# Optimization experiments

Hardware: AMD Instinct MI355X
Metric: run time of the kernel (lower is better)

The kernel has to match this reference:

```python
import jax, jax.numpy as jnp
import numpy as np

D_MODEL = 1024
N_HEADS = 16
HEAD_DIM = D_MODEL // N_HEADS


def setup_inputs() -> dict:
    key = jax.random.key(0)
    ks = jax.random.split(key, 5)
    x = jax.random.normal(ks[0], (4, 2048, D_MODEL), dtype=jnp.float32)
    s = 1.0 / np.sqrt(D_MODEL)
    W_qkv = jax.random.normal(ks[1], (D_MODEL, 3 * D_MODEL), dtype=jnp.float32) * s
    b_qkv = jnp.zeros((3 * D_MODEL,), dtype=jnp.float32)
    W_proj = jax.random.normal(ks[2], (D_MODEL, D_MODEL), dtype=jnp.float32) * s
    b_proj = jnp.zeros((D_MODEL,), dtype=jnp.float32)
    return {"x": x, "W_qkv": W_qkv, "b_qkv": b_qkv, "W_proj": W_proj, "b_proj": b_proj}


def reference(x, W_qkv, b_qkv, W_proj, b_proj):
    B, T, C = x.shape
    H, Dh = N_HEADS, HEAD_DIM
    qkv = x @ W_qkv + b_qkv                      # [B,T,3C]
    q, k, v = jnp.split(qkv, 3, axis=-1)
    # [B,T,C] -> [B,H,T,Dh]
    q = q.reshape(B, T, H, Dh).transpose(0, 2, 1, 3)
    k = k.reshape(B, T, H, Dh).transpose(0, 2, 1, 3)
    v = v.reshape(B, T, H, Dh).transpose(0, 2, 1, 3)
    scale = 1.0 / np.sqrt(Dh)
    att = jnp.einsum("bhqd,bhkd->bhqk", q, k) * scale
    causal = jnp.tril(jnp.ones((T, T), dtype=bool))
    att = jnp.where(causal, att, -jnp.inf)
    att = jax.nn.softmax(att, axis=-1)
    y = jnp.einsum("bhqk,bhkd->bhqd", att, v)    # [B,H,T,Dh]
    y = y.transpose(0, 2, 1, 3).reshape(B, T, C)
    return y @ W_proj + b_proj
```

## Files before the change

kernel.cpp:

```cpp
#include <hip/hip_runtime.h>
#include <hip/hip_bf16.h>
#include <cstdint>
#include <math.h>

#define DM   1024
#define NH   16
#define DH   64
#define BB   4
#define TT   2048
#define MTOT (BB*TT)

using short8 = __attribute__((ext_vector_type(8))) short;
using f32x4  = __attribute__((ext_vector_type(4))) float;

__device__ __forceinline__ f32x4 mfma16(short8 a, short8 b, f32x4 c) {
  return __builtin_amdgcn_mfma_f32_16x16x32_bf16(a, b, c, 0, 0, 0);
}

typedef const __attribute__((address_space(1))) unsigned int* as1_u32p;
typedef __attribute__((address_space(3))) unsigned int*       as3_u32p;

__device__ __forceinline__ void gl_lds16(const void* g, void* l) {
  __builtin_amdgcn_global_load_lds(
      (as1_u32p)(reinterpret_cast<uintptr_t>(g)),
      (as3_u32p)((unsigned int)(reinterpret_cast<uintptr_t>(l))),
      16, 0, 0);
}

__device__ __forceinline__ int swz64(int row, int col) {
  return row*64 + ((((col >> 3) ^ (row & 7)) << 3) | (col & 7));
}

__device__ __forceinline__ unsigned pkbf(float a, float b) {
  __hip_bfloat162 h = __float22bfloat162_rn(make_float2(a, b));
  return *reinterpret_cast<unsigned*>(&h);
}

__device__ __forceinline__ void perm16p(unsigned &a, unsigned &b) {
  asm("v_permlane16_swap_b32 %0, %1" : "+v"(a), "+v"(b));
}
__device__ __forceinline__ void perm32p(unsigned &a, unsigned &b) {
  asm("v_permlane32_swap_b32 %0, %1" : "+v"(a), "+v"(b));
}

__device__ __forceinline__ short8 ldsr_o0(unsigned a) {
  short8 r; asm volatile("ds_read_b128 %0, %1" : "=v"(r) : "v"(a)); return r;
}
__device__ __forceinline__ short8 ldsr_o1(unsigned a) {
  short8 r; asm volatile("ds_read_b128 %0, %1 offset:2048" : "=v"(r) : "v"(a)); return r;
}
__device__ __forceinline__ short8 ldsr_o2(unsigned a) {
  short8 r; asm volatile("ds_read_b128 %0, %1 offset:4096" : "=v"(r) : "v"(a)); return r;
}
__device__ __forceinline__ short8 ldsr_o3(unsigned a) {
  short8 r; asm volatile("ds_read_b128 %0, %1 offset:6144" : "=v"(r) : "v"(a)); return r;
}
__device__ __forceinline__ short8 ldsr_o4(unsigned a) {
  short8 r; asm volatile("ds_read_b128 %0, %1 offset:8192" : "=v"(r) : "v"(a)); return r;
}
__device__ __forceinline__ short8 ldsr_o5(unsigned a) {
  short8 r; asm volatile("ds_read_b128 %0, %1 offset:10240" : "=v"(r) : "v"(a)); return r;
}

#define LGKM0  do { asm volatile("s_waitcnt lgkmcnt(0)"); __builtin_amdgcn_sched_barrier(0); } while(0)
#define VMCNT6 do { __builtin_amdgcn_sched_barrier(0); asm volatile("s_waitcnt vmcnt(6)"); __builtin_amdgcn_sched_barrier(0); } while(0)
#define VMCNT0 do { __builtin_amdgcn_sched_barrier(0); asm volatile("s_waitcnt vmcnt(0)"); __builtin_amdgcn_sched_barrier(0); } while(0)
#define BARRIER do { __builtin_amdgcn_s_barrier(); __builtin_amdgcn_sched_barrier(0); } while(0)

__global__ __launch_bounds__(256) void k_cvt(const float* __restrict__ in,
                                             __hip_bfloat16* __restrict__ out, int n8) {
  int i = blockIdx.x * 256 + threadIdx.x;
  if (i >= n8) return;
  const float* p = in + (size_t)i * 8;
  short8 o;
#pragma unroll
  for (int j = 0; j < 8; ++j) {
    __hip_bfloat16 h = __float2bfloat16(p[j]);
    o[j] = *reinterpret_cast<short*>(&h);
  }
  *reinterpret_cast<short8*>(out + (size_t)i * 8) = o;
}

__global__ __launch_bounds__(256) void k_transpose_cvt(const float* __restrict__ W,
                                                       __hip_bfloat16* __restrict__ Wt,
                                                       int K, int N) {
  __shared__ float tbuf[32][33];
  const int n0 = blockIdx.x * 32, k0 = blockIdx.y * 32;
  const int tx = threadIdx.x & 31, ty = threadIdx.x >> 5;
#pragma unroll
  for (int i = 0; i < 4; ++i)
    tbuf[ty + i*8][tx] = W[(size_t)(k0 + ty + i*8) * N + n0 + tx];
  __syncthreads();
#pragma unroll
  for (int i = 0; i < 4; ++i)
    Wt[(size_t)(n0 + ty + i*8) * K + k0 + tx] = __float2bfloat16(tbuf[tx][ty + i*8]);
}

__global__ __launch_bounds__(512, 2) void k_gemm3(const __hip_bfloat16* __restrict__ A,
                                                  const __hip_bfloat16* __restrict__ Bt,
                                                  const float* __restrict__ bias,
                                                  __hip_bfloat16* __restrict__ Qb,
                                                  __hip_bfloat16* __restrict__ Kb,
                                                  __hip_bfloat16* __restrict__ Vtb) {
  __shared__ __hip_bfloat16 As[2][256 * 64];
  __shared__ __hip_bfloat16 Bs[2][192 * 64];
  const int tid = threadIdx.x;
  const int l = tid & 63, w = tid >> 6;
  const int lr = l & 15, lg = l >> 4;
  const int wm = w >> 1, wn = w & 1;
  const int m0 = blockIdx.x * 256, n0 = blockIdx.y * 192;

  const int srow = tid >> 3;
  const int scol = (((tid & 7) ^ (srow & 7)) << 3);
  const size_t aoffs = (size_t)(m0 + srow) * 1024 + scol;
  const size_t boffs = (size_t)(n0 + srow) * 1024 + scol;
  const int ldst = tid * 8;

  auto stage = [&](int t, int s) {
    const int k0 = t * 64;
#pragma unroll
    for (int rd = 0; rd < 4; ++rd)
      gl_lds16(A + aoffs + (size_t)rd * 65536 + k0, &As[s][rd * 4096 + ldst]);
#pragma unroll
    for (int rd = 0; rd < 3; ++rd)
      gl_lds16(Bt + boffs + (size_t)rd * 65536 + k0, &Bs[s][rd * 4096 + ldst]);
  };

  const unsigned asLds = (unsigned)(uintptr_t)&As[0][0];
  const unsigned bsLds = (unsigned)(uintptr_t)&Bs[0][0];
  const unsigned aBase0 = asLds + 2u * ((wm*64 + lr) * 64 + ((lg ^ (lr & 7)) << 3));
  const unsigned bBase0 = bsLds + 2u * ((wn*96 + lr) * 64 + ((lg ^ (lr & 7)) << 3));

  stage(0, 0);
  VMCNT0;
  BARRIER;

  f32x4 acc[4][6] = {};
  short8 a_[4][2], b_[3][2];

#pragma unroll
  for (int t = 0; t < 16; ++t) {
    const int s = t & 1;
    const unsigned aB0 = aBase0 + (unsigned)s * 32768u;
    const unsigned aB1 = aB0 ^ 64u;
    const unsigned bB0 = bBase0 + (unsigned)s * 24576u;
    const unsigned bB1 = bB0 ^ 64u;
    if (t < 15) stage(t + 1, s ^ 1);
    a_[0][0] = ldsr_o0(aB0); a_[1][0] = ldsr_o1(aB0); a_[2][0] = ldsr_o2(aB0); a_[3][0] = ldsr_o3(aB0);
    a_[0][1] = ldsr_o0(aB1); a_[1][1] = ldsr_o1(aB1); a_[2][1] = ldsr_o2(aB1); a_[3][1] = ldsr_o3(aB1);
    b_[0][0] = ldsr_o0(bB0); b_[1][0] = ldsr_o1(bB0); b_[2][0] = ldsr_o2(bB0);
    b_[0][1] = ldsr_o0(bB1); b_[1][1] = ldsr_o1(bB1); b_[2][1] = ldsr_o2(bB1);
    LGKM0;
    __builtin_amdgcn_s_setprio(1);
#pragma unroll
    for (int m = 0; m < 4; ++m)
#pragma unroll
      for (int n = 0; n < 3; ++n)
#pragma unroll
        for (int ks = 0; ks < 2; ++ks)
          acc[m][n] = mfma16(a_[m][ks], b_[n][ks], acc[m][n]);
    __builtin_amdgcn_s_setprio(0);
    b_[0][0] = ldsr_o3(bB0); b_[1][0] = ldsr_o4(bB0); b_[2][0] = ldsr_o5(bB0);
    b_[0][1] = ldsr_o3(bB1); b_[1][1] = ldsr_o4(bB1); b_[2][1] = ldsr_o5(bB1);
    LGKM0;
    __builtin_amdgcn_s_setprio(1);
#pragma unroll
    for (int m = 0; m < 4; ++m)
#pragma unroll
      for (int n = 0; n < 3; ++n)
#pragma unroll
        for (int ks = 0; ks < 2; ++ks)
          acc[m][n + 3] = mfma16(a_[m][ks], b_[n][ks], acc[m][n + 3]);
    __builtin_amdgcn_s_setprio(0);
    if (t < 15) { VMCNT0; }
    BARRIER;
  }

  __syncthreads();
  __hip_bfloat16* reg = (w < 4) ? (&As[0][0] + w * 6144)
                                : (&Bs[0][0] + (w - 4) * 6144);
  const int colbase = n0 + wn * 96;
  const int rowbase = m0 + wm * 64;
  const int bidx = rowbase >> 11;
  const int tbase = rowbase & 2047;
  const float qs = 0.18033688011112042f;
  float bv[6];
#pragma unroll
  for (int g = 0; g < 6; ++g) bv[g] = bias[colbase + g * 16 + lr];
#pragma unroll
  for (int g = 0; g < 6; ++g) {
    const int cg0 = colbase + g * 16;
    const int which = cg0 >> 10;
    __hip_bfloat16* rg = reg + g * 1024;
    if (which == 2) {
#pragma unroll
      for (int m = 0; m < 4; ++m)
#pragma unroll
        for (int r = 0; r < 4; ++r) {
          const int t = m * 16 + lg * 4 + r;
          rg[lr * 64 + (t ^ ((lr & 7) << 3))] = __float2bfloat16(acc[m][g][r] + bv[g]);
        }
    } else {
      const float sc = (which == 0) ? qs : 1.f;
#pragma unroll
      for (int m = 0; m < 4; ++m)
#pragma unroll
        for (int r = 0; r < 4; ++r) {
          const int t = m * 16 + lg * 4 + r;
          rg[t * 16 + (lr ^ (((t >> 2) & 1) << 3))] =
              __float2bfloat16((acc[m][g][r] + bv[g]) * sc);
        }
    }
  }
#pragma unroll
  for (int g = 0; g < 6; ++g) {
    const int cg0 = colbase + g * 16;
    const int which = cg0 >> 10;
    const int hh = (cg0 >> 6) & 15;
    const int dd0 = cg0 & 48;
    const size_t bh = (size_t)bidx * 16 + hh;
    const __hip_bfloat16* rg = reg + g * 1024;
    if (which < 2) {
      __hip_bfloat16* basep = (which == 0) ? Qb : Kb;
      const int t = l;
      const int Xc = ((t >> 2) & 1) << 3;
      short8 y0 = *reinterpret_cast<const short8*>(&rg[t * 16 + Xc]);
      short8 y1 = *reinterpret_cast<const short8*>(&rg[t * 16 + (Xc ^ 8)]);
      __hip_bfloat16* dst = basep + (bh * TT + tbase + t) * 64 + dd0;
      *reinterpret_cast<short8*>(dst) = y0;
      *reinterpret_cast<short8*>(dst + 8) = y1;
    } else {
      const int dd = l >> 2, tseg = l & 3;
      const int X = (dd & 7) << 3;
      const int S0 = (((tseg ^ (X >> 4)) & 3) << 4) | (X & 8);
      short8 y0 = *reinterpret_cast<const short8*>(&rg[dd * 64 + S0]);
      short8 y1 = *reinterpret_cast<const short8*>(&rg[dd * 64 + (S0 ^ 8)]);
      __hip_bfloat16* dst = Vtb + (bh * 64 + dd0 + dd) * TT + tbase + tseg * 16;
      *reinterpret_cast<short8*>(dst) = y0;
      *reinterpret_cast<short8*>(dst + 8) = y1;
    }
  }
}

__global__ __launch_bounds__(512, 2) void k_gemm2(const __hip_bfloat16* __restrict__ A,
                                                  const __hip_bfloat16* __restrict__ Bt,
                                                  const float* __restrict__ bias,
                                                  float* __restrict__ outF) {
  __shared__ __hip_bfloat16 As[3][256 * 64];
  __shared__ __hip_bfloat16 Bs[3][128 * 64];
  const int tid = threadIdx.x;
  const int l = tid & 63, w = tid >> 6;
  const int lr = l & 15, lg = l >> 4;
  const int wm = w >> 1, wn = w & 1;
  const int m0 = blockIdx.x * 256, n0 = blockIdx.y * 128;

  const int srow = tid >> 3;
  const int scol = (((tid & 7) ^ (srow & 7)) << 3);
  const size_t aoffs = (size_t)(m0 + srow) * 1024 + scol;
  const size_t boffs = (size_t)(n0 + srow) * 1024 + scol;
  const int ldst = tid * 8;

  auto stage = [&](int t, int s) {
    const int k0 = t * 64;
    __hip_bfloat16* as_ = &As[s][0];
    __hip_bfloat16* bs_ = &Bs[s][0];
#pragma unroll
    for (int rd = 0; rd < 4; ++rd)
      gl_lds16(A + aoffs + (size_t)rd * 65536 + k0, as_ + rd * 4096 + ldst);
#pragma unroll
    for (int rd = 0; rd < 2; ++rd)
      gl_lds16(Bt + boffs + (size_t)rd * 65536 + k0, bs_ + rd * 4096 + ldst);
  };

  const unsigned asLds = (unsigned)(uintptr_t)&As[0][0];
  const unsigned bsLds = (unsigned)(uintptr_t)&Bs[0][0];
  const unsigned aBase = asLds + 2u * ((wm*64 + lr) * 64 + ((lg ^ (lr & 7)) << 3));
  const unsigned bBase = bsLds + 2u * ((wn*64 + lr) * 64 + ((lg ^ (lr & 7)) << 3));

  stage(0, 0);
  stage(1, 1);
  VMCNT6;
  BARRIER;

  f32x4 acc[4][4] = {};
  short8 a_[4][2], b_[2][2];

#pragma unroll
  for (int t = 0; t < 16; ++t) {
    const int s = t % 3;
    const unsigned aB0 = aBase + (unsigned)s * 32768u;
    const unsigned aB1 = aB0 ^ 64u;
    const unsigned bB0 = bBase + (unsigned)s * 16384u;
    const unsigned bB1 = bB0 ^ 64u;
    if (t + 2 < 16) stage(t + 2, (t + 2) % 3);
    a_[0][0] = ldsr_o0(aB0); a_[1][0] = ldsr_o1(aB0); a_[2][0] = ldsr_o2(aB0); a_[3][0] = ldsr_o3(aB0);
    a_[0][1] = ldsr_o0(aB1); a_[1][1] = ldsr_o1(aB1); a_[2][1] = ldsr_o2(aB1); a_[3][1] = ldsr_o3(aB1);
    b_[0][0] = ldsr_o0(bB0); b_[1][0] = ldsr_o1(bB0);
    b_[0][1] = ldsr_o0(bB1); b_[1][1] = ldsr_o1(bB1);
    LGKM0;
    __builtin_amdgcn_s_setprio(1);
#pragma unroll
    for (int m = 0; m < 4; ++m)
#pragma unroll
      for (int n = 0; n < 2; ++n)
#pragma unroll
        for (int ks = 0; ks < 2; ++ks)
          acc[m][n] = mfma16(a_[m][ks], b_[n][ks], acc[m][n]);
    __builtin_amdgcn_s_setprio(0);
    b_[0][0] = ldsr_o2(bB0); b_[1][0] = ldsr_o3(bB0);
    b_[0][1] = ldsr_o2(bB1); b_[1][1] = ldsr_o3(bB1);
    LGKM0;
    __builtin_amdgcn_s_setprio(1);
#pragma unroll
    for (int m = 0; m < 4; ++m)
#pragma unroll
      for (int n = 0; n < 2; ++n)
#pragma unroll
        for (int ks = 0; ks < 2; ++ks)
          acc[m][n + 2] = mfma16(a_[m][ks], b_[n][ks], acc[m][n + 2]);
    __builtin_amdgcn_s_setprio(0);
    if (t <= 13) { VMCNT6; }
    else if (t == 14) { VMCNT0; }
    BARRIER;
  }

  __syncthreads();
#pragma unroll
  for (int n = 0; n < 4; ++n) {
    const int col = n0 + wn * 64 + n * 16 + lr;
    const float bvv = bias[col];
#pragma unroll
    for (int m = 0; m < 4; ++m)
#pragma unroll
      for (int r = 0; r < 4; ++r) {
        const int row = m0 + wm * 64 + m * 16 + lg * 4 + r;
        outF[(size_t)row * 1024 + col] = acc[m][n][r] + bvv;
      }
  }
}

__device__ __forceinline__ void tile_step(f32x4 s0, f32x4 s1, int kbase, int kmaxw, int qmb,
                                          short8 v0, short8 v1, short8 v2, short8 v3,
                                          f32x4 (&acc)[4], float& lrun) {
  if (kbase + 31 > kmaxw - 15) {
#pragma unroll
    for (int r = 0; r < 4; ++r) {
      const int off = (r & 1) + ((r & 2) << 2);
      if (kbase + off > qmb)      s0[r] = -INFINITY;
      if (kbase + 16 + off > qmb) s1[r] = -INFINITY;
    }
  }
  float p0 = __builtin_amdgcn_exp2f(s0[0]), p1 = __builtin_amdgcn_exp2f(s0[1]);
  float p2 = __builtin_amdgcn_exp2f(s0[2]), p3 = __builtin_amdgcn_exp2f(s0[3]);
  float p4 = __builtin_amdgcn_exp2f(s1[0]), p5 = __builtin_amdgcn_exp2f(s1[1]);
  float p6 = __builtin_amdgcn_exp2f(s1[2]), p7 = __builtin_amdgcn_exp2f(s1[3]);
  lrun += ((p0 + p1) + (p2 + p3)) + ((p4 + p5) + (p6 + p7));
  unsigned u0 = pkbf(p0, p1);
  unsigned u1 = pkbf(p2, p3);
  unsigned u2 = pkbf(p4, p5);
  unsigned u3 = pkbf(p6, p7);
  perm16p(u0, u1);
  perm16p(u2, u3);
  perm32p(u0, u2);
  perm32p(u1, u3);
  union { unsigned u[4]; short8 s; } pw;
  pw.u[0] = u0; pw.u[1] = u2; pw.u[2] = u1; pw.u[3] = u3;
  const short8 pf = pw.s;
  acc[0] = mfma16(v0, pf, acc[0]);
  acc[1] = mfma16(v1, pf, acc[1]);
  acc[2] = mfma16(v2, pf, acc[2]);
  acc[3] = mfma16(v3, pf, acc[3]);
}

__device__ __forceinline__ void store_tile(__hip_bfloat16* Ylds, f32x4 (&acc)[4],
                                           float lrun, int q0, int w, int l,
                                           int lr, int lg, int bh,
                                           __hip_bfloat16* __restrict__ Y) {
  lrun += __shfl_xor(lrun, 16);
  lrun += __shfl_xor(lrun, 32);
  const float inv = 1.f / lrun;
#pragma unroll
  for (int nb = 0; nb < 4; ++nb) {
#pragma unroll
    for (int r = 0; r < 4; ++r) {
      const int d = nb * 16 + lg * 4 + r;
      Ylds[swz64(lr, d)] = __float2bfloat16(acc[nb][r] * inv);
    }
  }
  const int rr = l >> 2, part = l & 3;
  const int trow = q0 + w * 16 + rr;
  const int b = bh >> 4, h = bh & 15;
  short8 y0 = *reinterpret_cast<const short8*>(&Ylds[swz64(rr, part * 16)]);
  short8 y1 = *reinterpret_cast<const short8*>(&Ylds[swz64(rr, part * 16 + 8)]);
  __hip_bfloat16* dst = Y + ((size_t)b * TT + trow) * 1024 + h * 64 + part * 16;
  *reinterpret_cast<short8*>(dst) = y0;
  *reinterpret_cast<short8*>(dst + 8) = y1;
}

__global__ __launch_bounds__(256, 4) void k_flash(const __hip_bfloat16* __restrict__ Qb,
                                                  const __hip_bfloat16* __restrict__ Kb,
                                                  const __hip_bfloat16* __restrict__ Vtb,
                                                  __hip_bfloat16* __restrict__ Y) {
  __shared__ __hip_bfloat16 Klds[128 * 64];
  __shared__ __hip_bfloat16 Vtlds[64 * 128];
  const int tid = threadIdx.x;
  const int l = tid & 63, w = tid >> 6;
  const int lr = l & 15, lg = l >> 4;
  const int p  = blockIdx.x >> 6;
  const int bh = blockIdx.x & 63;
  const int q0A = p * 64, q0B = (31 - p) * 64;
  const __hip_bfloat16* Qp = Qb + (size_t)bh * TT * 64;
  const __hip_bfloat16* Kp = Kb + (size_t)bh * TT * 64;
  const __hip_bfloat16* Vp = Vtb + (size_t)bh * 64 * TT;
  const int qrowA = q0A + w * 16 + lr;
  const int qrowB = q0B + w * 16 + lr;
  const short8 qfA0 = *reinterpret_cast<const short8*>(Qp + (size_t)qrowA * 64 + lg * 8);
  const short8 qfA1 = *reinterpret_cast<const short8*>(Qp + (size_t)qrowA * 64 + 32 + lg * 8);
  const short8 qfB0 = *reinterpret_cast<const short8*>(Qp + (size_t)qrowB * 64 + lg * 8);
  const short8 qfB1 = *reinterpret_cast<const short8*>(Qp + (size_t)qrowB * 64 + 32 + lg * 8);
  f32x4 accA[4] = {}, accB[4] = {};
  float lA = 0.f, lB = 0.f;

  const int ka  = lr * 64 + ((lg ^ (lr & 7)) << 3);
  const int va  = lr * 128 + ((lg ^ (lr & 15)) << 3);

  const __hip_bfloat16* gk[4];
  const __hip_bfloat16* gv[4];
  __hip_bfloat16* lk[4];
  __hip_bfloat16* lv[4];
#pragma unroll
  for (int it = 0; it < 4; ++it) {
    int e = it * 2048 + tid * 8;
    int rowk = e >> 6;
    int lcolk = ((((e >> 3) & 7) ^ (rowk & 7)) << 3);
    int rk = rowk & 15;
    int srk = (((rk >> 1) ^ (rk >> 3)) & 1) ? (rk ^ 10) : rk;
    int rowks = (rowk & ~15) | srk;
    gk[it] = Kp + (size_t)rowks * 64 + lcolk;
    lk[it] = &Klds[e];
    int rowv = e >> 7;
    int lcolv = ((((e >> 3) & 15) ^ (rowv & 15)) << 3);
    gv[it] = Vp + (size_t)rowv * TT + lcolv;
    lv[it] = &Vtlds[e];
  }

  const int kmaxwA = q0A + w * 16 + 15;
  const int kmaxwB = q0B + w * 16 + 15;
  const int base_lg = ((lg & 1) << 2) | (lg & 2);
  const int qmbA = qrowA - base_lg;
  const int qmbB = qrowB - base_lg;
  const int nblk = (q0B + 63) / 128 + 1;
  for (int blk = 0; blk < nblk; ++blk) {
    const int kv0 = blk * 128;
#pragma unroll
    for (int it = 0; it < 4; ++it) {
      gl_lds16(gk[it], lk[it]);
      gk[it] += 128 * 64;
    }
#pragma unroll
    for (int it = 0; it < 4; ++it) {
      gl_lds16(gv[it], lv[it]);
      gv[it] += 128;
    }
    __syncthreads();
#pragma unroll
    for (int kci = 0; kci < 4; ++kci) {
      const int kbase = kv0 + kci * 32;
      if (kbase > kmaxwB) break;
      const int kb = ka + kci * 2048;
      const short8 kf00 = *reinterpret_cast<const short8*>(&Klds[kb]);
      const short8 kf10 = *reinterpret_cast<const short8*>(&Klds[kb + 1024]);
      const short8 kf01 = *reinterpret_cast<const short8*>(&Klds[kb ^ 32]);
      const short8 kf11 = *reinterpret_cast<const short8*>(&Klds[(kb + 1024) ^ 32]);
      f32x4 sB0 = {}, sB1 = {};
      sB0 = mfma16(kf00, qfB0, sB0);
      sB1 = mfma16(kf10, qfB0, sB1);
      sB0 = mfma16(kf01, qfB1, sB0);
      sB1 = mfma16(kf11, qfB1, sB1);
      const bool aAct = (kbase <= kmaxwA);
      f32x4 sA0 = {}, sA1 = {};
      if (aAct) {
        sA0 = mfma16(kf00, qfA0, sA0);
        sA1 = mfma16(kf10, qfA0, sA1);
        sA0 = mfma16(kf01, qfA1, sA0);
        sA1 = mfma16(kf11, qfA1, sA1);
      }
      const int vb = va ^ (kci * 32);
      const short8 v0 = *reinterpret_cast<const short8*>(&Vtlds[vb]);
      const short8 v1 = *reinterpret_cast<const short8*>(&Vtlds[vb + 2048]);
      const short8 v2 = *reinterpret_cast<const short8*>(&Vtlds[vb + 4096]);
      const short8 v3 = *reinterpret_cast<const short8*>(&Vtlds[vb + 6144]);
      tile_step(sB0, sB1, kbase, kmaxwB, qmbB, v0, v1, v2, v3, accB, lB);
      if (aAct)
        tile_step(sA0, sA1, kbase, kmaxwA, qmbA, v0, v1, v2, v3, accA, lA);
    }
    __syncthreads();
  }
  __hip_bfloat16* Ylds = Klds + w * 1024;
  store_tile(Ylds, accA, lA, q0A, w, l, lr, lg, bh, Y);
  store_tile(Ylds, accB, lB, q0B, w, l, lr, lg, bh, Y);
}

extern "C" void kernel_launch(void* const* d_in, const int* in_sizes, int n_in,
                              void* d_out, int out_size, void* d_ws, size_t ws_size,
                              hipStream_t stream) {
  const float* x     = (const float*)d_in[0];
  const float* Wqkv  = (const float*)d_in[1];
  const float* bqkv  = (const float*)d_in[2];
  const float* Wproj = (const float*)d_in[3];
  const float* bproj = (const float*)d_in[4];

  char* ws = (char*)d_ws;
  size_t off = 0;
  auto alloc = [&](size_t bytes) {
    char* p = ws + off;
    off += (bytes + 255) & ~(size_t)255;
    return p;
  };
  __hip_bfloat16* xb    = (__hip_bfloat16*)alloc((size_t)MTOT * 1024 * 2);
  __hip_bfloat16* wqkvT = (__hip_bfloat16*)alloc((size_t)3072 * 1024 * 2);
  __hip_bfloat16* wpT   = (__hip_bfloat16*)alloc((size_t)1024 * 1024 * 2);
  __hip_bfloat16* Qb    = (__hip_bfloat16*)alloc((size_t)64 * TT * 64 * 2);
  __hip_bfloat16* Kb    = (__hip_bfloat16*)alloc((size_t)64 * TT * 64 * 2);
  __hip_bfloat16* Vtb   = (__hip_bfloat16*)alloc((size_t)64 * TT * 64 * 2);
  __hip_bfloat16* Yb    = (__hip_bfloat16*)alloc((size_t)MTOT * 1024 * 2);

  k_cvt<<<(MTOT * 1024 / 8 + 255) / 256, 256, 0, stream>>>(x, xb, MTOT * 1024 / 8);
  k_transpose_cvt<<<dim3(3072 / 32, 1024 / 32), 256, 0, stream>>>(Wqkv, wqkvT, 1024, 3072);
  k_transpose_cvt<<<dim3(1024 / 32, 1024 / 32), 256, 0, stream>>>(Wproj, wpT, 1024, 1024);
  k_gemm3<<<dim3(32, 16), 512, 0, stream>>>(xb, wqkvT, bqkv, Qb, Kb, Vtb);
  k_flash<<<16 * 64, 256, 0, stream>>>(Qb, Kb, Vtb, Yb);
  k_gemm2<<<dim3(32, 8), 512, 0, stream>>>(Yb, wpT, bproj, (float*)d_out);
}
```

Measured before the change: 147.1 us.

## Double-buffer K/V tiles in flash kernel and swizzle GEMM block order

The flash attention kernel now double-buffers the K and V^T LDS tiles, prefetching the next block with async global-to-LDS loads while the current block is computed. Partial vmcnt waits and explicit ds_read_b128 with lgkmcnt waits replace the full syncthreads drain. LDS use doubles, so launch bounds drop from 4 to 2 blocks per CU, which lowers occupancy. Both GEMM kernels also remap block indices into a swizzled order meant to improve L2 reuse of the operand tiles.

```diff
diff --git a/kernel.cpp b/kernel.cpp
--- a/kernel.cpp
+++ b/kernel.cpp
@@ -61,8 +61,13 @@
 __device__ __forceinline__ short8 ldsr_o5(unsigned a) {
   short8 r; asm volatile("ds_read_b128 %0, %1 offset:10240" : "=v"(r) : "v"(a)); return r;
 }
+__device__ __forceinline__ short8 ldsr_o6(unsigned a) {
+  short8 r; asm volatile("ds_read_b128 %0, %1 offset:12288" : "=v"(r) : "v"(a)); return r;
+}
 
 #define LGKM0  do { asm volatile("s_waitcnt lgkmcnt(0)"); __builtin_amdgcn_sched_barrier(0); } while(0)
+#define LGKM4  do { asm volatile("s_waitcnt lgkmcnt(4)"); __builtin_amdgcn_sched_barrier(0); } while(0)
+#define VMCNT8 do { __builtin_amdgcn_sched_barrier(0); asm volatile("s_waitcnt vmcnt(8)"); __builtin_amdgcn_sched_barrier(0); } while(0)
 #define VMCNT6 do { __builtin_amdgcn_sched_barrier(0); asm volatile("s_waitcnt vmcnt(6)"); __builtin_amdgcn_sched_barrier(0); } while(0)
 #define VMCNT0 do { __builtin_amdgcn_sched_barrier(0); asm volatile("s_waitcnt vmcnt(0)"); __builtin_amdgcn_sched_barrier(0); } while(0)
 #define BARRIER do { __builtin_amdgcn_s_barrier(); __builtin_amdgcn_sched_barrier(0); } while(0)
@@ -108,7 +113,9 @@
   const int l = tid & 63, w = tid >> 6;
   const int lr = l & 15, lg = l >> 4;
   const int wm = w >> 1, wn = w & 1;
-  const int m0 = blockIdx.x * 256, n0 = blockIdx.y * 192;
+  const int lin = (int)blockIdx.x + ((int)blockIdx.y << 5);
+  const int swzb = (lin & 7) * 64 + (lin >> 3);
+  const int m0 = (swzb & 31) * 256, n0 = (swzb >> 5) * 192;
 
   const int srow = tid >> 3;
   const int scol = (((tid & 7) ^ (srow & 7)) << 3);
@@ -252,7 +259,9 @@
   const int l = tid & 63, w = tid >> 6;
   const int lr = l & 15, lg = l >> 4;
   const int wm = w >> 1, wn = w & 1;
-  const int m0 = blockIdx.x * 256, n0 = blockIdx.y * 128;
+  const int lin = (int)blockIdx.x + ((int)blockIdx.y << 5);
+  const int swzb = (lin & 7) * 32 + (lin >> 3);
+  const int m0 = (swzb & 31) * 256, n0 = (swzb >> 5) * 128;
 
   const int srow = tid >> 3;
   const int scol = (((tid & 7) ^ (srow & 7)) << 3);
@@ -397,12 +406,12 @@
   *reinterpret_cast<short8*>(dst + 8) = y1;
 }
 
-__global__ __launch_bounds__(256, 4) void k_flash(const __hip_bfloat16* __restrict__ Qb,
+__global__ __launch_bounds__(256, 2) void k_flash(const __hip_bfloat16* __restrict__ Qb,
                                                   const __hip_bfloat16* __restrict__ Kb,
                                                   const __hip_bfloat16* __restrict__ Vtb,
                                                   __hip_bfloat16* __restrict__ Y) {
-  __shared__ __hip_bfloat16 Klds[128 * 64];
-  __shared__ __hip_bfloat16 Vtlds[64 * 128];
+  __shared__ __hip_bfloat16 Klds[2][128 * 64];
+  __shared__ __hip_bfloat16 Vtlds[2][64 * 128];
   const int tid = threadIdx.x;
   const int l = tid & 63, w = tid >> 6;
   const int lr = l & 15, lg = l >> 4;
@@ -423,6 +432,8 @@
 
   const int ka  = lr * 64 + ((lg ^ (lr & 7)) << 3);
   const int va  = lr * 128 + ((lg ^ (lr & 15)) << 3);
+  const unsigned kaB = (unsigned)(uintptr_t)&Klds[0][0] + 2u * (unsigned)ka;
+  const unsigned vaB = (unsigned)(uintptr_t)&Vtlds[0][0] + 2u * (unsigned)va;
 
   const __hip_bfloat16* gk[4];
   const __hip_bfloat16* gv[4];
@@ -437,11 +448,11 @@
     int srk = (((rk >> 1) ^ (rk >> 3)) & 1) ? (rk ^ 10) : rk;
     int rowks = (rowk & ~15) | srk;
     gk[it] = Kp + (size_t)rowks * 64 + lcolk;
-    lk[it] = &Klds[e];
+    lk[it] = &Klds[0][e];
     int rowv = e >> 7;
     int lcolv = ((((e >> 3) & 15) ^ (rowv & 15)) << 3);
     gv[it] = Vp + (size_t)rowv * TT + lcolv;
-    lv[it] = &Vtlds[e];
+    lv[it] = &Vtlds[0][e];
   }
 
   const int kmaxwA = q0A + w * 16 + 15;
@@ -450,28 +461,42 @@
   const int qmbA = qrowA - base_lg;
   const int qmbB = qrowB - base_lg;
   const int nblk = (q0B + 63) / 128 + 1;
+
+#pragma unroll
+  for (int it = 0; it < 4; ++it) { gl_lds16(gk[it], lk[it]); gk[it] += 8192; }
+#pragma unroll
+  for (int it = 0; it < 4; ++it) { gl_lds16(gv[it], lv[it]); gv[it] += 128; }
+
   for (int blk = 0; blk < nblk; ++blk) {
     const int kv0 = blk * 128;
-#pragma unroll
-    for (int it = 0; it < 4; ++it) {
-      gl_lds16(gk[it], lk[it]);
-      gk[it] += 128 * 64;
+    const unsigned so = (unsigned)((blk & 1) << 14);
+    if (blk + 1 < nblk) {
+      const int sn = ((blk + 1) & 1) << 13;
+#pragma unroll
+      for (int it = 0; it < 4; ++it) { gl_lds16(gk[it], lk[it] + sn); gk[it] += 8192; }
+#pragma unroll
+      for (int it = 0; it < 4; ++it) { gl_lds16(gv[it], lv[it] + sn); gv[it] += 128; }
+      VMCNT8;
+    } else {
+      VMCNT0;
     }
-#pragma unroll
-    for (int it = 0; it < 4; ++it) {
-      gl_lds16(gv[it], lv[it]);
-      gv[it] += 128;
-    }
-    __syncthreads();
+    BARRIER;
 #pragma unroll
     for (int kci = 0; kci < 4; ++kci) {
       const int kbase = kv0 + kci * 32;
       if (kbase > kmaxwB) break;
-      const int kb = ka + kci * 2048;
-      const short8 kf00 = *reinterpret_cast<const short8*>(&Klds[kb]);
-      const short8 kf10 = *reinterpret_cast<const short8*>(&Klds[kb + 1024]);
-      const short8 kf01 = *reinterpret_cast<const short8*>(&Klds[kb ^ 32]);
-      const short8 kf11 = *reinterpret_cast<const short8*>(&Klds[(kb + 1024) ^ 32]);
+      const unsigned kA  = kaB + so + (unsigned)(kci * 4096);
+      const unsigned kAx = kA ^ 64u;
+      const unsigned vA  = (vaB + so) ^ (unsigned)(kci * 64);
+      const short8 kf00 = ldsr_o0(kA);
+      const short8 kf10 = ldsr_o1(kA);
+      const short8 kf01 = ldsr_o0(kAx);
+      const short8 kf11 = ldsr_o1(kAx);
+      const short8 v0 = ldsr_o0(vA);
+      const short8 v1 = ldsr_o2(vA);
+      const short8 v2 = ldsr_o4(vA);
+      const short8 v3 = ldsr_o6(vA);
+      LGKM4;
       f32x4 sB0 = {}, sB1 = {};
       sB0 = mfma16(kf00, qfB0, sB0);
       sB1 = mfma16(kf10, qfB0, sB1);
@@ -485,18 +510,14 @@
         sA0 = mfma16(kf01, qfA1, sA0);
         sA1 = mfma16(kf11, qfA1, sA1);
       }
-      const int vb = va ^ (kci * 32);
-      const short8 v0 = *reinterpret_cast<const short8*>(&Vtlds[vb]);
-      const short8 v1 = *reinterpret_cast<const short8*>(&Vtlds[vb + 2048]);
-      const short8 v2 = *reinterpret_cast<const short8*>(&Vtlds[vb + 4096]);
-      const short8 v3 = *reinterpret_cast<const short8*>(&Vtlds[vb + 6144]);
+      LGKM0;
       tile_step(sB0, sB1, kbase, kmaxwB, qmbB, v0, v1, v2, v3, accB, lB);
       if (aAct)
         tile_step(sA0, sA1, kbase, kmaxwA, qmbA, v0, v1, v2, v3, accA, lA);
     }
-    __syncthreads();
-  }
-  __hip_bfloat16* Ylds = Klds + w * 1024;
+    BARRIER;
+  }
+  __hip_bfloat16* Ylds = &Klds[0][0] + w * 1024;
   store_tile(Ylds, accA, lA, q0A, w, l, lr, lg, bh, Y);
   store_tile(Ylds, accB, lB, q0B, w, l, lr, lg, bh, Y);
 }
```

Measured after the change: 165.4 us. +12.4%, slower.

## Assign each wave one 32-row query strip instead of split A/B rows

Applied to the files above, without the earlier changes.

Before, every wave handled 16 rows from the low query tile (A) and 16 rows from the high tile (B). Now waves 0-1 own the 32 rows of tile A and waves 2-3 own the 32 rows of tile B. Each wave reuses the same K fragments for two adjacent 16-row score tiles. A-waves stop computing early but still join every block barrier, so the block's length is set by the B-waves, which now carry more work each. The lower 16-row subtile also computes one fully masked 32-key chunk near the diagonal.

```diff
diff --git a/kernel.cpp b/kernel.cpp
--- a/kernel.cpp
+++ b/kernel.cpp
@@ -373,7 +373,7 @@
 }
 
 __device__ __forceinline__ void store_tile(__hip_bfloat16* Ylds, f32x4 (&acc)[4],
-                                           float lrun, int q0, int w, int l,
+                                           float lrun, int rowbase, int l,
                                            int lr, int lg, int bh,
                                            __hip_bfloat16* __restrict__ Y) {
   lrun += __shfl_xor(lrun, 16);
@@ -388,7 +388,7 @@
     }
   }
   const int rr = l >> 2, part = l & 3;
-  const int trow = q0 + w * 16 + rr;
+  const int trow = rowbase + rr;
   const int b = bh >> 4, h = bh & 15;
   short8 y0 = *reinterpret_cast<const short8*>(&Ylds[swz64(rr, part * 16)]);
   short8 y1 = *reinterpret_cast<const short8*>(&Ylds[swz64(rr, part * 16 + 8)]);
@@ -409,17 +409,18 @@
   const int p  = blockIdx.x >> 6;
   const int bh = blockIdx.x & 63;
   const int q0A = p * 64, q0B = (31 - p) * 64;
+  const int q0w = ((w >> 1) ? q0B : q0A) + (w & 1) * 32;
   const __hip_bfloat16* Qp = Qb + (size_t)bh * TT * 64;
   const __hip_bfloat16* Kp = Kb + (size_t)bh * TT * 64;
   const __hip_bfloat16* Vp = Vtb + (size_t)bh * 64 * TT;
-  const int qrowA = q0A + w * 16 + lr;
-  const int qrowB = q0B + w * 16 + lr;
-  const short8 qfA0 = *reinterpret_cast<const short8*>(Qp + (size_t)qrowA * 64 + lg * 8);
-  const short8 qfA1 = *reinterpret_cast<const short8*>(Qp + (size_t)qrowA * 64 + 32 + lg * 8);
-  const short8 qfB0 = *reinterpret_cast<const short8*>(Qp + (size_t)qrowB * 64 + lg * 8);
-  const short8 qfB1 = *reinterpret_cast<const short8*>(Qp + (size_t)qrowB * 64 + 32 + lg * 8);
-  f32x4 accA[4] = {}, accB[4] = {};
-  float lA = 0.f, lB = 0.f;
+  const int qrow0 = q0w + lr;
+  const int qrow1 = q0w + 16 + lr;
+  const short8 qf00 = *reinterpret_cast<const short8*>(Qp + (size_t)qrow0 * 64 + lg * 8);
+  const short8 qf01 = *reinterpret_cast<const short8*>(Qp + (size_t)qrow0 * 64 + 32 + lg * 8);
+  const short8 qf10 = *reinterpret_cast<const short8*>(Qp + (size_t)qrow1 * 64 + lg * 8);
+  const short8 qf11 = *reinterpret_cast<const short8*>(Qp + (size_t)qrow1 * 64 + 32 + lg * 8);
+  f32x4 acc0[4] = {}, acc1[4] = {};
+  float l0 = 0.f, l1 = 0.f;
 
   const int ka  = lr * 64 + ((lg ^ (lr & 7)) << 3);
   const int va  = lr * 128 + ((lg ^ (lr & 15)) << 3);
@@ -444,11 +445,11 @@
     lv[it] = &Vtlds[e];
   }
 
-  const int kmaxwA = q0A + w * 16 + 15;
-  const int kmaxwB = q0B + w * 16 + 15;
+  const int kmaxw = q0w + 31;
+  const int kmax0 = q0w + 15;
   const int base_lg = ((lg & 1) << 2) | (lg & 2);
-  const int qmbA = qrowA - base_lg;
-  const int qmbB = qrowB - base_lg;
+  const int qmb0 = qrow0 - base_lg;
+  const int qmb1 = qrow1 - base_lg;
   const int nblk = (q0B + 63) / 128 + 1;
   for (int blk = 0; blk < nblk; ++blk) {
     const int kv0 = blk * 128;
@@ -466,39 +467,35 @@
 #pragma unroll
     for (int kci = 0; kci < 4; ++kci) {
       const int kbase = kv0 + kci * 32;
-      if (kbase > kmaxwB) break;
+      if (kbase > kmaxw) break;
       const int kb = ka + kci * 2048;
       const short8 kf00 = *reinterpret_cast<const short8*>(&Klds[kb]);
       const short8 kf10 = *reinterpret_cast<const short8*>(&Klds[kb + 1024]);
       const short8 kf01 = *reinterpret_cast<const short8*>(&Klds[kb ^ 32]);
       const short8 kf11 = *reinterpret_cast<const short8*>(&Klds[(kb + 1024) ^ 32]);
-      f32x4 sB0 = {}, sB1 = {};
-      sB0 = mfma16(kf00, qfB0, sB0);
-      sB1 = mfma16(kf10, qfB0, sB1);
-      sB0 = mfma16(kf01, qfB1, sB0);
-      sB1 = mfma16(kf11, qfB1, sB1);
-      const bool aAct = (kbase <= kmaxwA);
-      f32x4 sA0 = {}, sA1 = {};
-      if (aAct) {
-        sA0 = mfma16(kf00, qfA0, sA0);
-        sA1 = mfma16(kf10, qfA0, sA1);
-        sA0 = mfma16(kf01, qfA1, sA0);
-        sA1 = mfma16(kf11, qfA1, sA1);
-      }
       const int vb = va ^ (kci * 32);
       const short8 v0 = *reinterpret_cast<const short8*>(&Vtlds[vb]);
       const short8 v1 = *reinterpret_cast<const short8*>(&Vtlds[vb + 2048]);
       const short8 v2 = *reinterpret_cast<const short8*>(&Vtlds[vb + 4096]);
       const short8 v3 = *reinterpret_cast<const short8*>(&Vtlds[vb + 6144]);
-      tile_step(sB0, sB1, kbase, kmaxwB, qmbB, v0, v1, v2, v3, accB, lB);
-      if (aAct)
-        tile_step(sA0, sA1, kbase, kmaxwA, qmbA, v0, v1, v2, v3, accA, lA);
+      f32x4 s00 = {}, s01 = {};
+      s00 = mfma16(kf00, qf00, s00);
+      s01 = mfma16(kf10, qf00, s01);
+      s00 = mfma16(kf01, qf01, s00);
+      s01 = mfma16(kf11, qf01, s01);
+      f32x4 s10 = {}, s11 = {};
+      s10 = mfma16(kf00, qf10, s10);
+      s11 = mfma16(kf10, qf10, s11);
+      s10 = mfma16(kf01, qf11, s10);
+      s11 = mfma16(kf11, qf11, s11);
+      tile_step(s00, s01, kbase, kmax0, qmb0, v0, v1, v2, v3, acc0, l0);
+      tile_step(s10, s11, kbase, kmaxw, qmb1, v0, v1, v2, v3, acc1, l1);
     }
     __syncthreads();
   }
   __hip_bfloat16* Ylds = Klds + w * 1024;
-  store_tile(Ylds, accA, lA, q0A, w, l, lr, lg, bh, Y);
-  store_tile(Ylds, accB, lB, q0B, w, l, lr, lg, bh, Y);
+  store_tile(Ylds, acc0, l0, q0w,      l, lr, lg, bh, Y);
+  store_tile(Ylds, acc1, l1, q0w + 16, l, lr, lg, bh, Y);
 }
 
 extern "C" void kernel_launch(void* const* d_in, const int* in_sizes, int n_in,
```

New measurement: 154.7 us. 1.05x slower.

## Deepen QKV GEMM pipeline to four LDS stages with BK=32 tiles

Applied to the files above, without the earlier changes.

Rewrites the QKV projection GEMM main loop to use a four-slot LDS ring with K-step 32 and three stages in flight, instead of double buffering with K-step 64. Waits become partial vmcnt waits, so global loads for later stages stay outstanding during compute. The LDS layout and swizzle are redesigned to pack two 32-wide rows per 64-element line. This should hide global latency better, at the cost of twice as many barriers and loop iterations, more complex wait accounting, and a risk that the per-wave vmcnt thresholds are wrong.

```diff
diff --git a/kernel.cpp b/kernel.cpp
--- a/kernel.cpp
+++ b/kernel.cpp
@@ -55,15 +55,30 @@
 __device__ __forceinline__ short8 ldsr_o3(unsigned a) {
   short8 r; asm volatile("ds_read_b128 %0, %1 offset:6144" : "=v"(r) : "v"(a)); return r;
 }
-__device__ __forceinline__ short8 ldsr_o4(unsigned a) {
-  short8 r; asm volatile("ds_read_b128 %0, %1 offset:8192" : "=v"(r) : "v"(a)); return r;
-}
-__device__ __forceinline__ short8 ldsr_o5(unsigned a) {
-  short8 r; asm volatile("ds_read_b128 %0, %1 offset:10240" : "=v"(r) : "v"(a)); return r;
+__device__ __forceinline__ short8 ldsr_p0(unsigned a) {
+  short8 r; asm volatile("ds_read_b128 %0, %1" : "=v"(r) : "v"(a)); return r;
+}
+__device__ __forceinline__ short8 ldsr_p1(unsigned a) {
+  short8 r; asm volatile("ds_read_b128 %0, %1 offset:1024" : "=v"(r) : "v"(a)); return r;
+}
+__device__ __forceinline__ short8 ldsr_p2(unsigned a) {
+  short8 r; asm volatile("ds_read_b128 %0, %1 offset:2048" : "=v"(r) : "v"(a)); return r;
+}
+__device__ __forceinline__ short8 ldsr_p3(unsigned a) {
+  short8 r; asm volatile("ds_read_b128 %0, %1 offset:3072" : "=v"(r) : "v"(a)); return r;
+}
+__device__ __forceinline__ short8 ldsr_p4(unsigned a) {
+  short8 r; asm volatile("ds_read_b128 %0, %1 offset:4096" : "=v"(r) : "v"(a)); return r;
+}
+__device__ __forceinline__ short8 ldsr_p5(unsigned a) {
+  short8 r; asm volatile("ds_read_b128 %0, %1 offset:5120" : "=v"(r) : "v"(a)); return r;
 }
 
 #define LGKM0  do { asm volatile("s_waitcnt lgkmcnt(0)"); __builtin_amdgcn_sched_barrier(0); } while(0)
+#define VMCNT8 do { __builtin_amdgcn_sched_barrier(0); asm volatile("s_waitcnt vmcnt(8)"); __builtin_amdgcn_sched_barrier(0); } while(0)
 #define VMCNT6 do { __builtin_amdgcn_sched_barrier(0); asm volatile("s_waitcnt vmcnt(6)"); __builtin_amdgcn_sched_barrier(0); } while(0)
+#define VMCNT4 do { __builtin_amdgcn_sched_barrier(0); asm volatile("s_waitcnt vmcnt(4)"); __builtin_amdgcn_sched_barrier(0); } while(0)
+#define VMCNT3 do { __builtin_amdgcn_sched_barrier(0); asm volatile("s_waitcnt vmcnt(3)"); __builtin_amdgcn_sched_barrier(0); } while(0)
 #define VMCNT0 do { __builtin_amdgcn_sched_barrier(0); asm volatile("s_waitcnt vmcnt(0)"); __builtin_amdgcn_sched_barrier(0); } while(0)
 #define BARRIER do { __builtin_amdgcn_s_barrier(); __builtin_amdgcn_sched_barrier(0); } while(0)
 
@@ -102,83 +117,72 @@
                                                   __hip_bfloat16* __restrict__ Qb,
                                                   __hip_bfloat16* __restrict__ Kb,
                                                   __hip_bfloat16* __restrict__ Vtb) {
-  __shared__ __hip_bfloat16 As[2][256 * 64];
-  __shared__ __hip_bfloat16 Bs[2][192 * 64];
+  __shared__ __hip_bfloat16 Ls[4][14336];
   const int tid = threadIdx.x;
   const int l = tid & 63, w = tid >> 6;
   const int lr = l & 15, lg = l >> 4;
+  const int lr2 = lr >> 1;
   const int wm = w >> 1, wn = w & 1;
   const int m0 = blockIdx.x * 256, n0 = blockIdx.y * 192;
 
-  const int srow = tid >> 3;
-  const int scol = (((tid & 7) ^ (srow & 7)) << 3);
-  const size_t aoffs = (size_t)(m0 + srow) * 1024 + scol;
-  const size_t boffs = (size_t)(n0 + srow) * 1024 + scol;
-  const int ldst = tid * 8;
+  auto soff = [&](int e) {
+    const int rr = e >> 6;
+    const int c8 = ((e >> 3) & 7) ^ (rr & 7);
+    return (size_t)(rr * 2 + (c8 >> 2)) * 1024 + (c8 & 3) * 8;
+  };
+  const size_t aoff0 = (size_t)m0 * 1024 + soff(tid * 8);
+  const size_t aoff1 = (size_t)m0 * 1024 + soff(4096 + tid * 8);
+  const size_t boff0 = (size_t)n0 * 1024 + soff(tid * 8);
+  const size_t boff1 = (size_t)n0 * 1024 + soff(4096 + tid * 8);
+  const int ld0 = tid * 8;
+  const bool xb2 = (tid < 256);
 
   auto stage = [&](int t, int s) {
-    const int k0 = t * 64;
-#pragma unroll
-    for (int rd = 0; rd < 4; ++rd)
-      gl_lds16(A + aoffs + (size_t)rd * 65536 + k0, &As[s][rd * 4096 + ldst]);
-#pragma unroll
-    for (int rd = 0; rd < 3; ++rd)
-      gl_lds16(Bt + boffs + (size_t)rd * 65536 + k0, &Bs[s][rd * 4096 + ldst]);
+    const int kb = t * 32;
+    __hip_bfloat16* base = &Ls[s][0];
+    gl_lds16(A + aoff0 + kb, base + ld0);
+    gl_lds16(A + aoff1 + kb, base + 4096 + ld0);
+    gl_lds16(Bt + boff0 + kb, base + 8192 + ld0);
+    if (xb2) gl_lds16(Bt + boff1 + kb, base + 12288 + ld0);
   };
 
-  const unsigned asLds = (unsigned)(uintptr_t)&As[0][0];
-  const unsigned bsLds = (unsigned)(uintptr_t)&Bs[0][0];
-  const unsigned aBase0 = asLds + 2u * ((wm*64 + lr) * 64 + ((lg ^ (lr & 7)) << 3));
-  const unsigned bBase0 = bsLds + 2u * ((wn*96 + lr) * 64 + ((lg ^ (lr & 7)) << 3));
-
-  stage(0, 0);
-  VMCNT0;
+  const unsigned lsBase = (unsigned)(uintptr_t)&Ls[0][0];
+  const unsigned fslot = (unsigned)((((lr & 1) << 2) | lg) ^ (lr2 & 7));
+  const unsigned laneOff = (unsigned)(lr2 * 128) + fslot * 16u;
+  const unsigned aLane = lsBase + (unsigned)(wm * 4096) + laneOff;
+  const unsigned bLane = lsBase + 16384u + (unsigned)(wn * 6144) + laneOff;
+
+  stage(0, 0); stage(1, 1); stage(2, 2);
+  if (w < 4) { VMCNT8; } else { VMCNT6; }
   BARRIER;
 
   f32x4 acc[4][6] = {};
-  short8 a_[4][2], b_[3][2];
-
-#pragma unroll
-  for (int t = 0; t < 16; ++t) {
-    const int s = t & 1;
-    const unsigned aB0 = aBase0 + (unsigned)s * 32768u;
-    const unsigned aB1 = aB0 ^ 64u;
-    const unsigned bB0 = bBase0 + (unsigned)s * 24576u;
-    const unsigned bB1 = bB0 ^ 64u;
-    if (t < 15) stage(t + 1, s ^ 1);
-    a_[0][0] = ldsr_o0(aB0); a_[1][0] = ldsr_o1(aB0); a_[2][0] = ldsr_o2(aB0); a_[3][0] = ldsr_o3(aB0);
-    a_[0][1] = ldsr_o0(aB1); a_[1][1] = ldsr_o1(aB1); a_[2][1] = ldsr_o2(aB1); a_[3][1] = ldsr_o3(aB1);
-    b_[0][0] = ldsr_o0(bB0); b_[1][0] = ldsr_o1(bB0); b_[2][0] = ldsr_o2(bB0);
-    b_[0][1] = ldsr_o0(bB1); b_[1][1] = ldsr_o1(bB1); b_[2][1] = ldsr_o2(bB1);
+  short8 a_[4], b_[6];
+
+#pragma unroll 4
+  for (int t = 0; t < 32; ++t) {
+    const int s = t & 3;
+    const unsigned aB = aLane + (unsigned)s * 28672u;
+    const unsigned bB = bLane + (unsigned)s * 28672u;
+    if (t < 29) stage(t + 3, (t + 3) & 3);
+    a_[0] = ldsr_p0(aB); a_[1] = ldsr_p1(aB); a_[2] = ldsr_p2(aB); a_[3] = ldsr_p3(aB);
+    b_[0] = ldsr_p0(bB); b_[1] = ldsr_p1(bB); b_[2] = ldsr_p2(bB);
+    b_[3] = ldsr_p3(bB); b_[4] = ldsr_p4(bB); b_[5] = ldsr_p5(bB);
     LGKM0;
     __builtin_amdgcn_s_setprio(1);
 #pragma unroll
-    for (int m = 0; m < 4; ++m)
-#pragma unroll
-      for (int n = 0; n < 3; ++n)
-#pragma unroll
-        for (int ks = 0; ks < 2; ++ks)
-          acc[m][n] = mfma16(a_[m][ks], b_[n][ks], acc[m][n]);
+    for (int n = 0; n < 6; ++n)
+#pragma unroll
+      for (int m = 0; m < 4; ++m)
+        acc[m][n] = mfma16(a_[m], b_[n], acc[m][n]);
     __builtin_amdgcn_s_setprio(0);
-    b_[0][0] = ldsr_o3(bB0); b_[1][0] = ldsr_o4(bB0); b_[2][0] = ldsr_o5(bB0);
-    b_[0][1] = ldsr_o3(bB1); b_[1][1] = ldsr_o4(bB1); b_[2][1] = ldsr_o5(bB1);
-    LGKM0;
-    __builtin_amdgcn_s_setprio(1);
-#pragma unroll
-    for (int m = 0; m < 4; ++m)
-#pragma unroll
-      for (int n = 0; n < 3; ++n)
-#pragma unroll
-        for (int ks = 0; ks < 2; ++ks)
-          acc[m][n + 3] = mfma16(a_[m][ks], b_[n][ks], acc[m][n + 3]);
-    __builtin_amdgcn_s_setprio(0);
-    if (t < 15) { VMCNT0; }
-    BARRIER;
+    if (t <= 28)      { if (w < 4) { VMCNT8; } else { VMCNT6; } BARRIER; }
+    else if (t == 29) { if (w < 4) { VMCNT4; } else { VMCNT3; } BARRIER; }
+    else if (t == 30) { VMCNT0; BARRIER; }
   }
 
   __syncthreads();
-  __hip_bfloat16* reg = (w < 4) ? (&As[0][0] + w * 6144)
-                                : (&Bs[0][0] + (w - 4) * 6144);
+  __hip_bfloat16* reg = &Ls[0][0] + w * 6144;
   const int colbase = n0 + wn * 96;
   const int rowbase = m0 + wm * 64;
   const int bidx = rowbase >> 11;
```

Result: slower. 153.0 us (+4.0%).
